# Kernel optimization log

Hardware: AMD Instinct MI355X
Metric: run time of the kernel (lower is better)

## Reference

```python
import jax, jax.numpy as jnp
import numpy as np

D_MODEL = 1024
NUM_HEADS = 16
D_K = D_MODEL // NUM_HEADS


def setup_inputs() -> dict:
    key = jax.random.key(0)
    ks = jax.random.split(key, 11)
    B, S = 2, 2048
    scale = 1.0 / np.sqrt(D_MODEL)
    return {
        "Q": jax.random.normal(ks[0], (B, S, D_MODEL), jnp.float32),
        "K": jax.random.normal(ks[1], (B, S, D_MODEL), jnp.float32),
        "V": jax.random.normal(ks[2], (B, S, D_MODEL), jnp.float32),
        "Wq": jax.random.normal(ks[3], (D_MODEL, D_MODEL), jnp.float32) * scale,
        "bq": jnp.zeros((D_MODEL,), jnp.float32),
        "Wk": jax.random.normal(ks[4], (D_MODEL, D_MODEL), jnp.float32) * scale,
        "bk": jnp.zeros((D_MODEL,), jnp.float32),
        "Wv": jax.random.normal(ks[5], (D_MODEL, D_MODEL), jnp.float32) * scale,
        "bv": jnp.zeros((D_MODEL,), jnp.float32),
        "Wo": jax.random.normal(ks[6], (D_MODEL, D_MODEL), jnp.float32) * scale,
        "bo": jnp.zeros((D_MODEL,), jnp.float32),
    }


def reference(Q, K, V, Wq, bq, Wk, bk, Wv, bv, Wo, bo):
    B, S, _ = Q.shape
    # linear projections (torch Linear: x @ W.T + b)
    q = Q @ Wq.T + bq
    k = K @ Wk.T + bk
    v = V @ Wv.T + bv
    # split heads: [B, S, H, d_k] -> [B, H, S, d_k]
    q = q.reshape(B, S, NUM_HEADS, D_K).transpose(0, 2, 1, 3)
    k = k.reshape(B, S, NUM_HEADS, D_K).transpose(0, 2, 1, 3)
    v = v.reshape(B, S, NUM_HEADS, D_K).transpose(0, 2, 1, 3)
    # scaled dot-product attention, full [B, H, S, S] scores as in original
    scores = jnp.einsum("bhqd,bhkd->bhqk", q, k) / jnp.sqrt(jnp.float32(D_K))
    probs = jax.nn.softmax(scores, axis=-1)
    attn = jnp.einsum("bhqk,bhkd->bhqd", probs, v)
    # merge heads and output projection
    attn = attn.transpose(0, 2, 1, 3).reshape(B, S, D_MODEL)
    return attn @ Wo.T + bo
```

## Files before the change

kernel.cpp:

```cpp
#include <hip/hip_runtime.h>
#include <cstdint>
#include <cstddef>

#define D_MODEL 1024
#define NHEADS 16
#define DK 64
#define BATCH 2
#define SEQ 2048
#define MROWS 4096

using f32x4 = __attribute__((ext_vector_type(4))) float;
using f32x16 = __attribute__((ext_vector_type(16))) float;
using u16x8 = __attribute__((ext_vector_type(8))) unsigned short;
using u32x4 = __attribute__((ext_vector_type(4))) unsigned int;
using bf16x8 = __attribute__((ext_vector_type(8))) __bf16;

static __device__ __forceinline__ f32x4 mfma16(u16x8 a, u16x8 b, f32x4 c) {
    return __builtin_amdgcn_mfma_f32_16x16x32_bf16(
        __builtin_bit_cast(bf16x8, a), __builtin_bit_cast(bf16x8, b), c, 0, 0, 0);
}
static __device__ __forceinline__ f32x16 mfma32(u16x8 a, u16x8 b, f32x16 c) {
    return __builtin_amdgcn_mfma_f32_32x32x16_bf16(
        __builtin_bit_cast(bf16x8, a), __builtin_bit_cast(bf16x8, b), c, 0, 0, 0);
}

static __device__ __forceinline__ unsigned short f2b(float f) {
    unsigned int u = __float_as_uint(f);
    u += 0x7fffu + ((u >> 16) & 1u);
    return (unsigned short)(u >> 16);
}
static __device__ __forceinline__ unsigned int cvt_pk(float lo, float hi) {
    unsigned int r;
    asm("v_cvt_pk_bf16_f32 %0, %1, %2" : "=v"(r) : "v"(lo), "v"(hi));
    return r;
}
static __device__ __forceinline__ void plswap(unsigned int& a, unsigned int& b) {
    asm("v_permlane32_swap_b32 %0, %1" : "+v"(a), "+v"(b));
}
static __device__ __forceinline__ float fexp2(float x) {
#if __has_builtin(__builtin_amdgcn_exp2f)
    return __builtin_amdgcn_exp2f(x);
#else
    float r;
    asm("v_exp_f32 %0, %1" : "=v"(r) : "v"(x));
    return r;
#endif
}
static __device__ __forceinline__ void gll16(const void* g, void* l) {
    __builtin_amdgcn_global_load_lds(
        (const __attribute__((address_space(1))) void*)g,
        (__attribute__((address_space(3))) void*)l, 16, 0, 0);
}
#define SBAR() __builtin_amdgcn_s_barrier()
#define SCHED0() __builtin_amdgcn_sched_barrier(0)
#define WAITV(n) asm volatile("s_waitcnt vmcnt(" #n ")" ::: "memory")

__global__ __launch_bounds__(256) void cvt_flat_kernel(
    const float* __restrict__ w0, const float* __restrict__ w1,
    const float* __restrict__ w2, const float* __restrict__ w3,
    const float* __restrict__ a0, const float* __restrict__ a1,
    const float* __restrict__ a2,
    unsigned short* __restrict__ outW, unsigned short* __restrict__ outA,
    float scale0) {
    const int idx = (int)blockIdx.x * 256 + (int)threadIdx.x;
    const float* src;
    ushort4* dst;
    float scale = 1.0f;
    if (idx < 4 * 262144) {
        const float* ws[4] = {w0, w1, w2, w3};
        int m = idx >> 18;
        int off = idx & 262143;
        src = ws[m] + off * 4;
        dst = reinterpret_cast<ushort4*>(outW) + ((size_t)m << 18) + off;
        if (m == 0) scale = scale0;
    } else {
        int ai = idx - 4 * 262144;
        const float* as[3] = {a0, a1, a2};
        int m = ai >> 20;
        int off = ai & 1048575;
        src = as[m] + off * 4;
        dst = reinterpret_cast<ushort4*>(outA) + ((size_t)m << 20) + off;
    }
    float4 v = *reinterpret_cast<const float4*>(src);
    ushort4 o;
    o.x = f2b(v.x * scale);
    o.y = f2b(v.y * scale);
    o.z = f2b(v.z * scale);
    o.w = f2b(v.w * scale);
    *dst = o;
}


__global__ __launch_bounds__(256, 4) void gemm_qkv_kernel(
    const unsigned short* __restrict__ Abf,
    const unsigned short* __restrict__ W,
    unsigned short* __restrict__ qo, unsigned short* __restrict__ ko,
    unsigned short* __restrict__ vto,
    const float* __restrict__ b0, const float* __restrict__ b1, const float* __restrict__ b2,
    float qsc) {
    __shared__ __align__(16) char Ab[2][8192];
    __shared__ __align__(16) char Wb[2][8192];

    const int tid = threadIdx.x;
    const int lane = tid & 63;
    const int wid = tid >> 6;
    const int wr = wid >> 1, wc = wid & 1;
    const int g = (lane >> 4) & 3, l16 = lane & 15;

    const int logical = ((int)blockIdx.x & 7) * 96 + ((int)blockIdx.x >> 3);
    const int m = logical >> 8;
    const int rem = logical & 255;
    const int y = rem >> 3, xc = rem & 7;
    const int row0 = y * 128;
    const int arow0 = m * MROWS + row0;
    const int wrow0 = m * 1024 + xc * 128;

    const int sline = tid >> 3;
    const int sgl = (tid & 7) ^ (sline & 7);
    const int srow = sline * 2 + (sgl >> 2);
    const int skcol = (sgl & 3) * 8;

    auto stage = [&](int k0, int buf) {
        const char* a0 = (const char*)Abf + (size_t)(arow0 + srow) * 2048 + (size_t)(k0 + skcol) * 2;
        gll16(a0, Ab[buf] + wid * 1024);
        gll16(a0 + (size_t)64 * 2048, Ab[buf] + 4096 + wid * 1024);
        const char* w0 = (const char*)W + (size_t)(wrow0 + srow) * 2048 + (size_t)(k0 + skcol) * 2;
        gll16(w0, Wb[buf] + wid * 1024);
        gll16(w0 + (size_t)64 * 2048, Wb[buf] + 4096 + wid * 1024);
    };

    const int rswz = ((((l16 & 1) << 2) + g) ^ ((l16 >> 1) & 7)) << 4;
    const int abase = (wr * 32 + (l16 >> 1)) * 128 + rswz;
    const int bbase = (wc * 32 + (l16 >> 1)) * 128 + rswz;

    f32x4 acc[4][4] = {};
    stage(0, 0);

    for (int t = 0; t < 32; ++t) {
        if (t < 31) stage((t + 1) * 32, (t & 1) ^ 1);
        if (t < 31) WAITV(4);
        else WAITV(0);
        SCHED0();
        SBAR();
        SCHED0();
        u16x8 af[4], bf[4];
#pragma unroll
        for (int mi = 0; mi < 4; ++mi)
            af[mi] = *reinterpret_cast<const u16x8*>(Ab[t & 1] + abase + mi * 1024);
#pragma unroll
        for (int ni = 0; ni < 4; ++ni)
            bf[ni] = *reinterpret_cast<const u16x8*>(Wb[t & 1] + bbase + ni * 1024);
        __builtin_amdgcn_s_setprio(1);
#pragma unroll
        for (int mi = 0; mi < 4; ++mi)
#pragma unroll
            for (int ni = 0; ni < 4; ++ni)
                acc[mi][ni] = mfma16(af[mi], bf[ni], acc[mi][ni]);
        __builtin_amdgcn_s_setprio(0);
        SBAR();
        SCHED0();
    }

    const float* bias = (m == 0) ? b0 : ((m == 1) ? b1 : b2);
    const float bsc = (m == 0) ? qsc : 1.0f;
#pragma unroll
    for (int mi = 0; mi < 4; ++mi) {
#pragma unroll
        for (int ni = 0; ni < 4; ++ni) {
            int r = row0 + wr * 64 + mi * 16 + g * 4;
            int cl = xc * 128 + wc * 64 + ni * 16 + l16;
            float bv = bsc * bias[cl];
            if (m < 2) {
                unsigned short* outp = m ? ko : qo;
#pragma unroll
                for (int j = 0; j < 4; ++j)
                    outp[(size_t)(r + j) * 1024 + cl] = f2b(acc[mi][ni][j] + bv);
            } else {
                ushort4 o;
                o.x = f2b(acc[mi][ni][0] + bv);
                o.y = f2b(acc[mi][ni][1] + bv);
                o.z = f2b(acc[mi][ni][2] + bv);
                o.w = f2b(acc[mi][ni][3] + bv);
                *reinterpret_cast<ushort4*>(vto + (size_t)cl * MROWS + r) = o;
            }
        }
    }
}

__global__ __launch_bounds__(256, 4) void gemm_out_kernel(
    const unsigned short* __restrict__ Abf,
    const unsigned short* __restrict__ W,
    float* __restrict__ fo,
    const float* __restrict__ bias) {
    __shared__ __align__(16) char Ab[2][8192];
    __shared__ __align__(16) char Wb[2][4096];

    const int tid = threadIdx.x;
    const int lane = tid & 63;
    const int wid = tid >> 6;
    const int wr = wid >> 1, wc = wid & 1;
    const int g = (lane >> 4) & 3, l16 = lane & 15;

    const int logical = ((int)blockIdx.x & 7) * 64 + ((int)blockIdx.x >> 3);
    const int y = logical >> 4, xc = logical & 15;
    const int row0 = y * 128;
    const int wrow0 = xc * 64;

    const int sline = tid >> 3;
    const int sgl = (tid & 7) ^ (sline & 7);
    const int srow = sline * 2 + (sgl >> 2);
    const int skcol = (sgl & 3) * 8;

    auto stage = [&](int k0, int buf) {
        const char* a0 = (const char*)Abf + (size_t)(row0 + srow) * 2048 + (size_t)(k0 + skcol) * 2;
        gll16(a0, Ab[buf] + wid * 1024);
        gll16(a0 + (size_t)64 * 2048, Ab[buf] + 4096 + wid * 1024);
        const char* w0 = (const char*)W + (size_t)(wrow0 + srow) * 2048 + (size_t)(k0 + skcol) * 2;
        gll16(w0, Wb[buf] + wid * 1024);
    };

    const int rswz = ((((l16 & 1) << 2) + g) ^ ((l16 >> 1) & 7)) << 4;
    const int abase = (wr * 32 + (l16 >> 1)) * 128 + rswz;
    const int bbase = (wc * 16 + (l16 >> 1)) * 128 + rswz;

    f32x4 acc[4][2] = {};
    stage(0, 0);

    for (int t = 0; t < 32; ++t) {
        if (t < 31) stage((t + 1) * 32, (t & 1) ^ 1);
        if (t < 31) WAITV(3);
        else WAITV(0);
        SCHED0();
        SBAR();
        SCHED0();
        u16x8 af[4], bf[2];
#pragma unroll
        for (int mi = 0; mi < 4; ++mi)
            af[mi] = *reinterpret_cast<const u16x8*>(Ab[t & 1] + abase + mi * 1024);
#pragma unroll
        for (int ni = 0; ni < 2; ++ni)
            bf[ni] = *reinterpret_cast<const u16x8*>(Wb[t & 1] + bbase + ni * 1024);
        __builtin_amdgcn_s_setprio(1);
#pragma unroll
        for (int mi = 0; mi < 4; ++mi)
#pragma unroll
            for (int ni = 0; ni < 2; ++ni)
                acc[mi][ni] = mfma16(af[mi], bf[ni], acc[mi][ni]);
        __builtin_amdgcn_s_setprio(0);
        SBAR();
        SCHED0();
    }

#pragma unroll
    for (int mi = 0; mi < 4; ++mi) {
#pragma unroll
        for (int ni = 0; ni < 2; ++ni) {
            int r = row0 + wr * 64 + mi * 16 + g * 4;
            int cl = xc * 64 + wc * 32 + ni * 16 + l16;
            float bv = bias[cl];
#pragma unroll
            for (int j = 0; j < 4; ++j)
                fo[(size_t)(r + j) * 1024 + cl] = acc[mi][ni][j] + bv;
        }
    }
}

__global__ __launch_bounds__(512, 2) void attn_kernel(
    const unsigned short* __restrict__ qp,
    const unsigned short* __restrict__ kp,
    const unsigned short* __restrict__ vT,
    unsigned short* __restrict__ ao) {
    __shared__ __align__(16) char lds[49152];

    const int tid = threadIdx.x;
    const int lane = tid & 63;
    const int wid = tid >> 6;
    const int wq = wid & 1, wk = wid >> 1;
    const int l31 = lane & 31, hi = lane >> 5;

    const int logical = ((int)blockIdx.x & 7) * 128 + ((int)blockIdx.x >> 3);
    const int qtile = logical & 31;
    const int bh = logical >> 5;
    const int b = bh >> 4, h = bh & 15;
    const int ch = h * DK;
    const int q0 = b * SEQ + qtile * 64;

    const int klp = (tid >> 4) & 15;
    const int kgl = (tid & 15) ^ klp;
    const int krow2 = klp * 2 + (kgl >> 3);
    const int koct = kgl & 7;
    const char* ksrc0 = (const char*)kp +
        ((size_t)(b * SEQ + (tid >> 8) * 512 + krow2)) * 2048 + ch * 2 + koct * 16;
    const int vd = tid >> 4;
    const int vglog = (tid & 15) ^ (vd & 15);
    const char* vsrc0 = (const char*)vT +
        ((size_t)(ch + vd)) * (MROWS * 2) +
        ((size_t)(b * SEQ + (vglog >> 2) * 512 + (vglog & 3) * 8)) * 2;

    const char* qr = (const char*)qp + (size_t)(q0 + wq * 32 + l31) * 2048 + ch * 2;
    u16x8 qf[4];
#pragma unroll
    for (int t = 0; t < 4; ++t)
        qf[t] = *reinterpret_cast<const u16x8*>(qr + t * 32 + hi * 16);

    char* kbuf = lds;
    char* vbuf = lds + 16384;

    auto stageK = [&](int kt2) {
        gll16(ksrc0 + (size_t)kt2 * 65536, kbuf + wid * 1024);
        gll16(ksrc0 + (size_t)kt2 * 65536 + (size_t)1024 * 2048, kbuf + 8192 + wid * 1024);
    };
    auto stageV = [&](int kt2, int buf) {
        char* base = vbuf + (buf << 14);
        gll16(vsrc0 + kt2 * 64, base + wid * 1024);
        gll16(vsrc0 + (size_t)32 * (MROWS * 2) + kt2 * 64, base + 8192 + wid * 1024);
    };

    f32x16 acco[2] = {};
    float l0 = 0.f, l1 = 0.f, l2 = 0.f, l3 = 0.f;

    stageV(0, 0);
    stageK(0);
    for (int kt = 0; kt < 16; ++kt) {
        if (kt < 15) {
            stageV(kt + 1, (kt + 1) & 1);
            WAITV(2);
        } else {
            WAITV(0);
        }
        SCHED0();
        SBAR();
        SCHED0();

        f32x16 s = {};
        __builtin_amdgcn_s_setprio(1);
#pragma unroll
        for (int t = 0; t < 4; ++t) {
            u16x8 kf = *reinterpret_cast<const u16x8*>(
                kbuf + (wk * 16 + (l31 >> 1)) * 256 +
                (((((l31 & 1) << 3) + 2 * t + hi) ^ ((l31 >> 1) & 15)) << 4));
            s = mfma32(kf, qf[t], s);
        }
        __builtin_amdgcn_s_setprio(0);
        SBAR();
        SCHED0();
        if (kt < 15) stageK(kt + 1);

        float p[16];
#pragma unroll
        for (int r = 0; r < 16; r += 4) {
            p[r] = fexp2(s[r]);
            p[r + 1] = fexp2(s[r + 1]);
            p[r + 2] = fexp2(s[r + 2]);
            p[r + 3] = fexp2(s[r + 3]);
            l0 += p[r];
            l1 += p[r + 1];
            l2 += p[r + 2];
            l3 += p[r + 3];
        }
        unsigned int pf0[4], pf1[4];
#pragma unroll
        for (int i = 0; i < 2; ++i) {
            unsigned int a = cvt_pk(p[2 * i], p[2 * i + 1]);
            unsigned int bb = cvt_pk(p[4 + 2 * i], p[5 + 2 * i]);
            plswap(a, bb);
            pf0[i] = a;
            pf0[i + 2] = bb;
            unsigned int a2 = cvt_pk(p[8 + 2 * i], p[9 + 2 * i]);
            unsigned int b2 = cvt_pk(p[12 + 2 * i], p[13 + 2 * i]);
            plswap(a2, b2);
            pf1[i] = a2;
            pf1[i + 2] = b2;
        }

        const char* Vb = vbuf + ((kt & 1) << 14);
        __builtin_amdgcn_s_setprio(1);
#pragma unroll
        for (int t = 0; t < 2; ++t) {
            u32x4 wv = t ? u32x4{pf1[0], pf1[1], pf1[2], pf1[3]}
                         : u32x4{pf0[0], pf0[1], pf0[2], pf0[3]};
            u16x8 pfr = __builtin_bit_cast(u16x8, wv);
#pragma unroll
            for (int dt = 0; dt < 2; ++dt) {
                u16x8 vf = *reinterpret_cast<const u16x8*>(
                    Vb + (dt * 32 + l31) * 256 + (((wk * 4 + 2 * t + hi) ^ (l31 & 15)) << 4));
                acco[dt] = mfma32(vf, pfr, acco[dt]);
            }
        }
        __builtin_amdgcn_s_setprio(0);
        SBAR();
        SCHED0();
    }

    float Lh = ((l0 + l1) + (l2 + l3));
    Lh += __shfl_xor(Lh, 32);

    float* cmb = reinterpret_cast<float*>(lds);
    if (wk >= 2) {
        float* slot = cmb + (size_t)((((wk - 2) * 2 + wq) * 64) + lane) * 34;
#pragma unroll
        for (int dt = 0; dt < 2; ++dt)
#pragma unroll
            for (int mm = 0; mm < 8; ++mm)
                *reinterpret_cast<float2*>(slot + dt * 16 + 2 * mm) =
                    float2{acco[dt][2 * mm], acco[dt][2 * mm + 1]};
        slot[32] = Lh;
    }
    __syncthreads();
    if (wk < 2) {
        const float* s2 = cmb + (size_t)(((wk * 2 + wq) * 64) + lane) * 34;
#pragma unroll
        for (int dt = 0; dt < 2; ++dt)
#pragma unroll
            for (int mm = 0; mm < 8; ++mm) {
                float2 t2 = *reinterpret_cast<const float2*>(s2 + dt * 16 + 2 * mm);
                acco[dt][2 * mm] += t2.x;
                acco[dt][2 * mm + 1] += t2.y;
            }
        Lh += s2[32];
    }
    __syncthreads();
    if (wk == 1) {
        float* slot = cmb + (size_t)((wq * 64) + lane) * 34;
#pragma unroll
        for (int dt = 0; dt < 2; ++dt)
#pragma unroll
            for (int mm = 0; mm < 8; ++mm)
                *reinterpret_cast<float2*>(slot + dt * 16 + 2 * mm) =
                    float2{acco[dt][2 * mm], acco[dt][2 * mm + 1]};
        slot[32] = Lh;
    }
    __syncthreads();
    if (wk == 0) {
        const float* s2 = cmb + (size_t)((wq * 64) + lane) * 34;
#pragma unroll
        for (int dt = 0; dt < 2; ++dt)
#pragma unroll
            for (int mm = 0; mm < 8; ++mm) {
                float2 t2 = *reinterpret_cast<const float2*>(s2 + dt * 16 + 2 * mm);
                acco[dt][2 * mm] += t2.x;
                acco[dt][2 * mm + 1] += t2.y;
            }
        Lh += s2[32];
    }
    __syncthreads();

    if (wk == 0) {
        float rl = 1.0f / Lh;
        const int r7 = l31 & 7;
        const int rr = lane >> 1, half = lane & 1;
        const int rb7 = rr & 7;
#pragma unroll
        for (int dt = 0; dt < 2; ++dt) {
            char* ot = lds + 36864 + (wid * 2 + dt) * 2304;
#pragma unroll
            for (int mm = 0; mm < 4; ++mm) {
                uint2 pko;
                pko.x = cvt_pk(acco[dt][4 * mm] * rl, acco[dt][4 * mm + 1] * rl);
                pko.y = cvt_pk(acco[dt][4 * mm + 2] * rl, acco[dt][4 * mm + 3] * rl);
                *reinterpret_cast<uint2*>(ot + l31 * 72 + (((2 * mm + hi) ^ r7) << 3)) = pko;
            }
            uint2 t0 = *reinterpret_cast<const uint2*>(ot + rr * 72 + (((half * 4 + 0) ^ rb7) << 3));
            uint2 t1 = *reinterpret_cast<const uint2*>(ot + rr * 72 + (((half * 4 + 1) ^ rb7) << 3));
            uint2 t2 = *reinterpret_cast<const uint2*>(ot + rr * 72 + (((half * 4 + 2) ^ rb7) << 3));
            uint2 t3 = *reinterpret_cast<const uint2*>(ot + rr * 72 + (((half * 4 + 3) ^ rb7) << 3));
            unsigned short* dst = ao + (size_t)(q0 + wq * 32 + rr) * 1024 + ch + dt * 32 + half * 16;
            uint4 o0 = {t0.x, t0.y, t1.x, t1.y};
            uint4 o1 = {t2.x, t2.y, t3.x, t3.y};
            *reinterpret_cast<uint4*>(dst) = o0;
            *reinterpret_cast<uint4*>(dst + 8) = o1;
        }
    }
}

extern "C" void kernel_launch(void* const* d_in, const int* in_sizes, int n_in,
                              void* d_out, int out_size, void* d_ws, size_t ws_size,
                              hipStream_t stream) {
    const float* Q = (const float*)d_in[0];
    const float* K = (const float*)d_in[1];
    const float* V = (const float*)d_in[2];
    const float* Wq = (const float*)d_in[3];
    const float* bq = (const float*)d_in[4];
    const float* Wk = (const float*)d_in[5];
    const float* bk = (const float*)d_in[6];
    const float* Wv = (const float*)d_in[7];
    const float* bv = (const float*)d_in[8];
    const float* Wo = (const float*)d_in[9];
    const float* bo = (const float*)d_in[10];

    unsigned short* ws = (unsigned short*)d_ws;
    const size_t SZ = (size_t)MROWS * D_MODEL;
    const size_t WSZ = (size_t)D_MODEL * D_MODEL;
    unsigned short* bufW = ws;
    unsigned short* abf = bufW + 4 * WSZ;
    unsigned short* qp = abf + 3 * SZ;
    unsigned short* kp = qp + SZ;
    unsigned short* vT = kp + SZ;
    unsigned short* ao = vT + SZ;

    const float qscale = 0.125f * 1.44269504088896f;

    dim3 blk(256);
    cvt_flat_kernel<<<dim3(16384), blk, 0, stream>>>(Wq, Wk, Wv, Wo, Q, K, V, bufW, abf, qscale);

    gemm_qkv_kernel<<<dim3(768), blk, 0, stream>>>(abf, bufW, qp, kp, vT, bq, bk, bv, qscale);

    attn_kernel<<<dim3(1024), dim3(512), 0, stream>>>(qp, kp, vT, ao);

    gemm_out_kernel<<<dim3(512), blk, 0, stream>>>(ao, bufW + 3 * WSZ, (float*)d_out, bo);
}
```

Measured before the change: 121.4 us.

## Load K fragments directly from global into registers, dropping K LDS staging

Each wave now reads its K fragments straight from global memory into registers at the start of every key tile, instead of staging K through LDS with async loads. This removes the K LDS buffer and one block barrier per iteration, and shrinks the LDS allocation, which could allow higher occupancy. The output staging area is moved to the start of LDS to fit the smaller buffer. The trade-off is that global-load latency for K is now exposed inside the loop with no prefetch one tile ahead, and different waves may load overlapping K rows redundantly.

```diff
diff --git a/kernel.cpp b/kernel.cpp
--- a/kernel.cpp
+++ b/kernel.cpp
@@ -270,7 +270,7 @@
     const unsigned short* __restrict__ kp,
     const unsigned short* __restrict__ vT,
     unsigned short* __restrict__ ao) {
-    __shared__ __align__(16) char lds[49152];
+    __shared__ __align__(16) char lds[34816];
 
     const int tid = threadIdx.x;
     const int lane = tid & 63;
@@ -285,12 +285,8 @@
     const int ch = h * DK;
     const int q0 = b * SEQ + qtile * 64;
 
-    const int klp = (tid >> 4) & 15;
-    const int kgl = (tid & 15) ^ klp;
-    const int krow2 = klp * 2 + (kgl >> 3);
-    const int koct = kgl & 7;
-    const char* ksrc0 = (const char*)kp +
-        ((size_t)(b * SEQ + (tid >> 8) * 512 + krow2)) * 2048 + ch * 2 + koct * 16;
+    const char* kbase = (const char*)kp +
+        ((size_t)(b * SEQ + wk * 512 + l31)) * 2048 + ch * 2 + hi * 16;
     const int vd = tid >> 4;
     const int vglog = (tid & 15) ^ (vd & 15);
     const char* vsrc0 = (const char*)vT +
@@ -303,13 +299,7 @@
     for (int t = 0; t < 4; ++t)
         qf[t] = *reinterpret_cast<const u16x8*>(qr + t * 32 + hi * 16);
 
-    char* kbuf = lds;
-    char* vbuf = lds + 16384;
-
-    auto stageK = [&](int kt2) {
-        gll16(ksrc0 + (size_t)kt2 * 65536, kbuf + wid * 1024);
-        gll16(ksrc0 + (size_t)kt2 * 65536 + (size_t)1024 * 2048, kbuf + 8192 + wid * 1024);
-    };
+    char* vbuf = lds;
     auto stageV = [&](int kt2, int buf) {
         char* base = vbuf + (buf << 14);
         gll16(vsrc0 + kt2 * 64, base + wid * 1024);
@@ -320,12 +310,18 @@
     float l0 = 0.f, l1 = 0.f, l2 = 0.f, l3 = 0.f;
 
     stageV(0, 0);
-    stageK(0);
     for (int kt = 0; kt < 16; ++kt) {
+        u16x8 kreg[4];
+        const char* kb = kbase + (size_t)kt * 65536;
+#pragma unroll
+        for (int t = 0; t < 4; ++t)
+            kreg[t] = *reinterpret_cast<const u16x8*>(kb + t * 32);
         if (kt < 15) {
             stageV(kt + 1, (kt + 1) & 1);
+            SCHED0();
             WAITV(2);
         } else {
+            SCHED0();
             WAITV(0);
         }
         SCHED0();
@@ -335,16 +331,9 @@
         f32x16 s = {};
         __builtin_amdgcn_s_setprio(1);
 #pragma unroll
-        for (int t = 0; t < 4; ++t) {
-            u16x8 kf = *reinterpret_cast<const u16x8*>(
-                kbuf + (wk * 16 + (l31 >> 1)) * 256 +
-                (((((l31 & 1) << 3) + 2 * t + hi) ^ ((l31 >> 1) & 15)) << 4));
-            s = mfma32(kf, qf[t], s);
-        }
+        for (int t = 0; t < 4; ++t)
+            s = mfma32(kreg[t], qf[t], s);
         __builtin_amdgcn_s_setprio(0);
-        SBAR();
-        SCHED0();
-        if (kt < 15) stageK(kt + 1);
 
         float p[16];
 #pragma unroll
@@ -452,7 +441,7 @@
         const int rb7 = rr & 7;
 #pragma unroll
         for (int dt = 0; dt < 2; ++dt) {
-            char* ot = lds + 36864 + (wid * 2 + dt) * 2304;
+            char* ot = lds + (wid * 2 + dt) * 2304;
 #pragma unroll
             for (int mm = 0; mm < 4; ++mm) {
                 uint2 pko;
```

New measurement: 155.0 us. +27.6%, slower.
